# Kernel tuning notes

Measured on AMD Instinct MI355X. Metric: run time of the kernel, lower is better.

## Reference

```python
import jax, jax.numpy as jnp
import numpy as np

KH = KW = 9
BN_EPS = 1e-5


def conv3x3(x, w):
    # x: [B,Cin,H,W], w: [Cout,Cin,3,3], stride 1, padding 1
    return jax.lax.conv_general_dilated(
        x, w, window_strides=(1, 1), padding=((1, 1), (1, 1)),
        dimension_numbers=("NCHW", "OIHW", "NCHW"))


def cbr(x, w, bn):
    # bn: [4, C] rows = (gamma, beta, running_mean, running_var); inference-mode BN
    g, b, m, v = bn[0], bn[1], bn[2], bn[3]
    x = conv3x3(x, w)
    x = (x - m[:, None, None]) * (g[:, None, None] / jnp.sqrt(v[:, None, None] + BN_EPS)) + b[:, None, None]
    return jax.nn.relu(x)


def weighting(x, atten):
    # x: [B,C,H,W], atten: [B,H,W,KH*KW]
    # out[b,c,h,w] = sum_k atten[b,h,w,k] * x[b,c, h+dh(k), w+dw(k)]  (zero-padded window)
    B, C, H, W = x.shape
    patches = jax.lax.conv_general_dilated_patches(
        x, filter_shape=(KH, KW), window_strides=(1, 1),
        padding=((KH // 2, KH // 2), (KW // 2, KW // 2)))  # [B, C*KH*KW, H, W], channel-major
    patches = patches.reshape(B, C, KH * KW, H, W)
    return jnp.einsum("bckhw,bhwk->bchw", patches, atten)


def _make_params(key, fc_dim=1024):
    d4, d16 = fc_dim // 4, fc_dim // 16
    ks = jax.random.split(key, 16)
    def conv_w(k, co, ci):
        return jax.random.normal(k, (co, ci, 3, 3), jnp.float32) * (1.0 / np.sqrt(ci * 9))
    def bn(k, c):
        g = 1.0 + 0.1 * jax.random.normal(k, (c,), jnp.float32)
        return jnp.stack([g, jnp.zeros((c,)), jnp.zeros((c,)), jnp.ones((c,))])
    p = {}
    p["w1"], p["bn1"] = conv_w(ks[0], d4, fc_dim), bn(ks[1], d4)
    p["w2"], p["bn2"] = conv_w(ks[2], d16, d4), bn(ks[3], d16)
    p["w3"], p["bn3"] = conv_w(ks[4], d4, d16), bn(ks[5], d4)
    p["w4"], p["bn4"] = conv_w(ks[6], d4, fc_dim), bn(ks[7], d4)
    p["w5"], p["bn5"] = conv_w(ks[8], d4, d4), bn(ks[9], d4)
    p["fw1"] = jax.random.normal(ks[10], (10, d4), jnp.float32) * (1.0 / np.sqrt(d4))
    p["fb1"] = jnp.zeros((10,), jnp.float32)
    p["fw2"] = jax.random.normal(ks[11], (1, 10), jnp.float32) * (1.0 / np.sqrt(10))
    p["fb2"] = jnp.zeros((1,), jnp.float32)
    return p


def setup_inputs() -> dict:
    key = jax.random.key(0)
    k1, k2, k3, kp = jax.random.split(key, 4)
    B, fc_dim, H, W = 4, 1024, 64, 64
    inp = {
        "low_key": jax.random.normal(k1, (B, fc_dim, H, W), jnp.float32),
        "low_nonkey": jax.random.normal(k2, (B, fc_dim, H, W), jnp.float32),
        "local_atten": jax.random.uniform(k3, (B, H, W, KH * KW), jnp.float32),
    }
    inp.update(_make_params(kp, fc_dim))
    return inp


def reference(low_key, low_nonkey, local_atten,
              w1, bn1, w2, bn2, w3, bn3, w4, bn4, w5, bn5,
              fw1, fb1, fw2, fb2):
    x = cbr(low_key, w1, bn1)        # [B, 256, H, W]
    x = cbr(x, w2, bn2)              # [B, 64, H, W]
    x = weighting(x, local_atten)    # 9x9 local-attention weighted gather
    x = cbr(x, w3, bn3)              # [B, 256, H, W]
    y = cbr(low_nonkey, w4, bn4)     # [B, 256, H, W]
    out = cbr(x - y, w5, bn5)        # [B, 256, H, W]
    out = out.mean(axis=(2, 3))      # adaptive avg pool to 1x1 -> [B, 256]
    out = out @ fw1.T + fb1          # [B, 10]
    out = out @ fw2.T + fb2          # [B, 1]
    return out
```

## Files before the change

kernel.cpp:

```cpp
#include <hip/hip_runtime.h>
#include <math.h>

typedef _Float16 f16;
typedef f16 f16x4 __attribute__((ext_vector_type(4)));
typedef f16 f16x8 __attribute__((ext_vector_type(8)));
typedef float f32x4 __attribute__((ext_vector_type(4)));

#define NB 4

__global__ void __launch_bounds__(256)
wtrans_kernel(const float* __restrict__ w, f16* __restrict__ wt, int Co, int Cin) {
  int idx = blockIdx.x * 256 + threadIdx.x;
  int total = Co * Cin * 9;
  if (idx >= total) return;
  int ci = idx % Cin, t2 = idx / Cin;
  int co = t2 % Co, k = t2 / Co;
  wt[idx] = (f16)w[((size_t)co * Cin + ci) * 9 + k];
}

__global__ void __launch_bounds__(256)
nchw2nhwc(const float* __restrict__ in, f16* __restrict__ out) {
  __shared__ f16 s[64][66];
  const int t = threadIdx.x;
  const int bh = blockIdx.x, c0 = blockIdx.y * 64;
  const int b = bh >> 6, h = bh & 63;
  const int w = t & 63, cr = t >> 6;
  #pragma unroll
  for (int i = 0; i < 16; ++i) {
    int c = c0 + cr * 16 + i;
    s[cr * 16 + i][w] = (f16)in[(((size_t)b * 1024 + c) * 64 + h) * 64 + w];
  }
  __syncthreads();
  #pragma unroll
  for (int i = 0; i < 2; ++i) {
    int task = t + 256 * i;
    int oct = task & 7, w2 = task >> 3;
    f16x8 v;
    #pragma unroll
    for (int j = 0; j < 8; ++j) v[j] = s[oct * 8 + j][w2];
    *(f16x8*)(out + (((size_t)b * 64 + h) * 64 + w2) * 1024 + c0 + oct * 8) = v;
  }
}

__global__ void __launch_bounds__(256)
conv_mfma(const f16* __restrict__ in, const f16* __restrict__ in2,
          const f16* __restrict__ wt, const float* __restrict__ bn,
          f16* __restrict__ out, float* __restrict__ pacc,
          float* __restrict__ partial, int Cin, int Co, int kspl) {
  __shared__ __align__(16) f16 xs[6][66][40];
  __shared__ __align__(16) f16 ws[9][64][40];
  __shared__ float s_red[4][64];

  const int t = threadIdx.x;
  const int tile = blockIdx.x;
  const int b = tile >> 4;
  const int h0 = (tile & 15) * 4;
  const int co_blk = blockIdx.y * 64;
  const int ciBase = blockIdx.z * (Cin / kspl);
  const int NC = (Cin / kspl) >> 5;
  const int wid = t >> 6, lane = t & 63;
  const int l15 = lane & 15, lg = lane >> 4;
  const int koff = lg * 8;

  f32x4 acc[4][4];
  #pragma unroll
  for (int m = 0; m < 4; ++m)
    #pragma unroll
    for (int n = 0; n < 4; ++n)
      #pragma unroll
      for (int r = 0; r < 4; ++r) acc[m][n][r] = 0.f;

  const f16* inb = in + (size_t)b * Cin * 4096;
  const f16* inb2 = in2 ? in2 + (size_t)b * Cin * 4096 : nullptr;

  const int wS = t >> 2, octS = t & 3;
  f16x8 ireg[6], wreg[9];

  auto load_stage = [&](int ci0) {
    #pragma unroll
    for (int r = 0; r < 6; ++r) {
      int gh = h0 - 1 + r;
      f16x8 v = {};
      if ((unsigned)gh < 64u) {
        size_t off = ((size_t)gh * 64 + wS) * Cin + ci0 + octS * 8;
        v = *(const f16x8*)(inb + off);
        if (inb2) { f16x8 v2 = *(const f16x8*)(inb2 + off); v = v - v2; }
      }
      ireg[r] = v;
    }
    #pragma unroll
    for (int i = 0; i < 9; ++i) {
      int s = t + 256 * i;
      int oct = s & 3, co = (s >> 2) & 63, k = s >> 8;
      wreg[i] = *(const f16x8*)(wt + ((size_t)k * Co + co_blk + co) * Cin + ci0 + oct * 8);
    }
  };
  auto write_stage = [&]() {
    #pragma unroll
    for (int r = 0; r < 6; ++r)
      *(f16x8*)&xs[r][wS + 1][octS * 8] = ireg[r];
    #pragma unroll
    for (int i = 0; i < 9; ++i) {
      int s = t + 256 * i;
      int oct = s & 3, co = (s >> 2) & 63, k = s >> 8;
      *(f16x8*)&ws[k][co][oct * 8] = wreg[i];
    }
  };

  if (t < 48) {
    int r = t >> 3, side = (t >> 2) & 1, oc = t & 3;
    f16x8 z = {};
    *(f16x8*)&xs[r][side * 65][oc * 8] = z;
  }
  load_stage(ciBase);
  write_stage();
  __syncthreads();

  for (int c = 0; c < NC; ++c) {
    if (c + 1 < NC) load_stage(ciBase + ((c + 1) << 5));
    #pragma unroll
    for (int tap = 0; tap < 9; ++tap) {
      const int dh = tap / 3 - 1, dw = tap % 3 - 1;
      f16x8 af[4];
      #pragma unroll
      for (int m = 0; m < 4; ++m)
        af[m] = *(const f16x8*)&ws[tap][m * 16 + l15][koff];
      #pragma unroll
      for (int n = 0; n < 4; ++n) {
        const f16x8 bf = *(const f16x8*)&xs[wid + dh + 1][n * 16 + l15 + 1 + dw][koff];
        #pragma unroll
        for (int m = 0; m < 4; ++m)
          acc[m][n] = __builtin_amdgcn_mfma_f32_16x16x32_f16(af[m], bf, acc[m][n], 0, 0, 0);
      }
    }
    __syncthreads();
    if (c + 1 < NC) write_stage();
    __syncthreads();
  }

  if (pacc) {
    float* pb = pacc + (size_t)blockIdx.z * 4194304 + (size_t)b * 4096 * Co;
    #pragma unroll
    for (int m = 0; m < 4; ++m)
      #pragma unroll
      for (int n = 0; n < 4; ++n) {
        int px = (h0 + wid) * 64 + n * 16 + l15;
        *(f32x4*)(pb + (size_t)px * Co + co_blk + m * 16 + lg * 4) = acc[m][n];
      }
  } else if (out) {
    #pragma unroll
    for (int m = 0; m < 4; ++m) {
      float sc[4], sh[4];
      #pragma unroll
      for (int reg = 0; reg < 4; ++reg) {
        int co = co_blk + m * 16 + lg * 4 + reg;
        sc[reg] = bn[co] / sqrtf(bn[3 * Co + co] + 1e-5f);
        sh[reg] = bn[Co + co] - bn[2 * Co + co] * sc[reg];
      }
      #pragma unroll
      for (int n = 0; n < 4; ++n) {
        f16x4 v;
        #pragma unroll
        for (int reg = 0; reg < 4; ++reg)
          v[reg] = (f16)fmaxf(fmaf(acc[m][n][reg], sc[reg], sh[reg]), 0.f);
        *(f16x4*)(out + ((size_t)(b * 64 + h0 + wid) * 64 + n * 16 + l15) * Co
                      + co_blk + m * 16 + lg * 4) = v;
      }
    }
  } else {
    #pragma unroll
    for (int m = 0; m < 4; ++m)
      #pragma unroll
      for (int reg = 0; reg < 4; ++reg) {
        int co = co_blk + m * 16 + lg * 4 + reg;
        float sc = bn[co] / sqrtf(bn[3 * Co + co] + 1e-5f);
        float sh = bn[Co + co] - bn[2 * Co + co] * sc;
        float s = 0.f;
        #pragma unroll
        for (int n = 0; n < 4; ++n)
          s += fmaxf(fmaf(acc[m][n][reg], sc, sh), 0.f);
        s += __shfl_xor(s, 1, 64);
        s += __shfl_xor(s, 2, 64);
        s += __shfl_xor(s, 4, 64);
        s += __shfl_xor(s, 8, 64);
        if (l15 == 0) s_red[wid][m * 16 + lg * 4 + reg] = s;
      }
    __syncthreads();
    if (t < 64) {
      float v = s_red[0][t] + s_red[1][t] + s_red[2][t] + s_red[3][t];
      partial[((size_t)b * Co + co_blk + t) * 16 + (tile & 15)] = v;
    }
  }
}

__global__ void __launch_bounds__(256)
kreduce(const float* __restrict__ pacc, const float* __restrict__ bn,
        f16* __restrict__ out, int Co) {
  const int t = threadIdx.x;
  const int coq = t & 63;
  float sc[4], sh[4];
  #pragma unroll
  for (int r = 0; r < 4; ++r) {
    int co = coq * 4 + r;
    sc[r] = bn[co] / sqrtf(bn[3 * Co + co] + 1e-5f);
    sh[r] = bn[Co + co] - bn[2 * Co + co] * sc[r];
  }
  #pragma unroll
  for (int i = 0; i < 4; ++i) {
    size_t idx = (size_t)blockIdx.x * 1024 + i * 256 + t;
    f32x4 a = *(const f32x4*)(pacc + idx * 4);
    f32x4 b2 = *(const f32x4*)(pacc + 4194304 + idx * 4);
    f16x4 v;
    #pragma unroll
    for (int r = 0; r < 4; ++r)
      v[r] = (f16)fmaxf(fmaf(a[r] + b2[r], sc[r], sh[r]), 0.f);
    *(f16x4*)(out + idx * 4) = v;
  }
}

__global__ void __launch_bounds__(256)
weighting_nhwc(const f16* __restrict__ x, const float* __restrict__ atten,
               f16* __restrict__ out) {
  __shared__ float s_a[64 * 81];
  const int h = blockIdx.x, b = blockIdx.y;
  const int t = threadIdx.x;
  for (int idx = t; idx < 64 * 81; idx += 256)
    s_a[idx] = atten[(size_t)((b * 64 + h) * 64) * 81 + idx];
  __syncthreads();

  const int w = t & 63, cg = t >> 6;
  float acc[16];
  #pragma unroll
  for (int j = 0; j < 16; ++j) acc[j] = 0.f;

  for (int dh = -4; dh <= 4; ++dh) {
    int hh = h + dh;
    if ((unsigned)hh >= 64u) continue;
    #pragma unroll
    for (int dw = -4; dw <= 4; ++dw) {
      int ww = w + dw;
      if ((unsigned)ww >= 64u) continue;
      float a = s_a[w * 81 + (dh + 4) * 9 + (dw + 4)];
      const f16* xp = x + (((size_t)b * 64 + hh) * 64 + ww) * 64 + cg * 16;
      f16x8 v0 = *(const f16x8*)xp;
      f16x8 v1 = *(const f16x8*)(xp + 8);
      #pragma unroll
      for (int j = 0; j < 8; ++j) {
        acc[j]     = fmaf(a, (float)v0[j], acc[j]);
        acc[8 + j] = fmaf(a, (float)v1[j], acc[8 + j]);
      }
    }
  }
  f16x8 o0, o1;
  #pragma unroll
  for (int j = 0; j < 8; ++j) { o0[j] = (f16)acc[j]; o1[j] = (f16)acc[8 + j]; }
  f16* op = out + (((size_t)b * 64 + h) * 64 + w) * 64 + cg * 16;
  *(f16x8*)op = o0;
  *(f16x8*)(op + 8) = o1;
}

__global__ void __launch_bounds__(256)
fc_kernel(const float* __restrict__ partial, const float* __restrict__ fw1,
          const float* __restrict__ fb1, const float* __restrict__ fw2,
          const float* __restrict__ fb2, float* __restrict__ outp) {
  const int t = threadIdx.x;
  const int b = t >> 6, lane = t & 63;
  float pooled[4];
  #pragma unroll
  for (int k = 0; k < 4; ++k) {
    int c = lane + 64 * k;
    float s = 0.f;
    #pragma unroll
    for (int p = 0; p < 16; ++p) s += partial[(size_t)(b * 256 + c) * 16 + p];
    pooled[k] = s * (1.f / 4096.f);
  }
  float o = 0.f;
  for (int i = 0; i < 10; ++i) {
    float d = 0.f;
    #pragma unroll
    for (int k = 0; k < 4; ++k) d += pooled[k] * fw1[i * 256 + lane + 64 * k];
    #pragma unroll
    for (int off = 32; off > 0; off >>= 1) d += __shfl_down(d, off, 64);
    o += (d + fb1[i]) * fw2[i];
  }
  if (lane == 0) outp[b] = o + fb2[0];
}

extern "C" void kernel_launch(void* const* d_in, const int* in_sizes, int n_in,
                              void* d_out, int out_size, void* d_ws, size_t ws_size,
                              hipStream_t stream) {
  const float* low_key    = (const float*)d_in[0];
  const float* low_nonkey = (const float*)d_in[1];
  const float* atten      = (const float*)d_in[2];
  const float* w1 = (const float*)d_in[3];  const float* bn1 = (const float*)d_in[4];
  const float* w2 = (const float*)d_in[5];  const float* bn2 = (const float*)d_in[6];
  const float* w3 = (const float*)d_in[7];  const float* bn3 = (const float*)d_in[8];
  const float* w4 = (const float*)d_in[9];  const float* bn4 = (const float*)d_in[10];
  const float* w5 = (const float*)d_in[11]; const float* bn5 = (const float*)d_in[12];
  const float* fw1 = (const float*)d_in[13]; const float* fb1 = (const float*)d_in[14];
  const float* fw2 = (const float*)d_in[15]; const float* fb2 = (const float*)d_in[16];

  f16* T   = (f16*)d_ws;
  f16* X1  = T + 16777216;
  f16* X2  = X1 + 4194304;
  f16* X3  = X2 + 1048576;
  f16* Y   = X3 + 1048576;
  f16* wt1 = Y + 4194304;
  f16* wt2 = wt1 + 2359296;
  f16* wt3 = wt2 + 147456;
  f16* wt4 = wt3 + 147456;
  f16* wt5 = wt4 + 2359296;
  float* P    = (float*)(wt5 + 589824);
  float* Pacc = P + 16384;

  dim3 blk(256);
  wtrans_kernel<<<(256 * 1024 * 9 + 255) / 256, blk, 0, stream>>>(w1, wt1, 256, 1024);
  wtrans_kernel<<<(64 * 256 * 9 + 255) / 256, blk, 0, stream>>>(w2, wt2, 64, 256);
  wtrans_kernel<<<(256 * 64 * 9 + 255) / 256, blk, 0, stream>>>(w3, wt3, 256, 64);
  wtrans_kernel<<<(256 * 1024 * 9 + 255) / 256, blk, 0, stream>>>(w4, wt4, 256, 1024);
  wtrans_kernel<<<(256 * 256 * 9 + 255) / 256, blk, 0, stream>>>(w5, wt5, 256, 256);

  nchw2nhwc<<<dim3(256, 16), blk, 0, stream>>>(low_key, T);
  conv_mfma<<<dim3(64, 4, 2), blk, 0, stream>>>(T, nullptr, wt1, bn1, nullptr, Pacc, nullptr, 1024, 256, 2);
  kreduce<<<1024, blk, 0, stream>>>(Pacc, bn1, X1, 256);
  conv_mfma<<<dim3(64, 1, 1), blk, 0, stream>>>(X1, nullptr, wt2, bn2, X2, nullptr, nullptr, 256, 64, 1);
  weighting_nhwc<<<dim3(64, NB), blk, 0, stream>>>(X2, atten, X3);
  conv_mfma<<<dim3(64, 4, 1), blk, 0, stream>>>(X3, nullptr, wt3, bn3, X1, nullptr, nullptr, 64, 256, 1);
  nchw2nhwc<<<dim3(256, 16), blk, 0, stream>>>(low_nonkey, T);
  conv_mfma<<<dim3(64, 4, 2), blk, 0, stream>>>(T, nullptr, wt4, bn4, nullptr, Pacc, nullptr, 1024, 256, 2);
  kreduce<<<1024, blk, 0, stream>>>(Pacc, bn4, Y, 256);
  conv_mfma<<<dim3(64, 4, 1), blk, 0, stream>>>(X1, Y, wt5, bn5, nullptr, nullptr, P, 256, 256, 1);
  fc_kernel<<<1, 256, 0, stream>>>(P, fw1, fb1, fw2, fb2, (float*)d_out);
}
```

Before: 337.6 us.

## Add larger-tile split-K conv kernel for 1024-channel convs and split-K conv2

Adds a 512-thread conv kernel for the two 1024-input-channel convolutions. Each block covers 128 output channels by 8 rows and the input channels are split four ways, so each shared-memory stage is reused across more MFMAs. The 256-to-64 conv, which previously launched only 64 blocks, is also split four ways with a partial-sum reduction. kreduce is generalised to any number of slabs, and the workspace is re-laid out so the partial buffers alias the X2/X3 region. The cost is more fp32 partial-sum traffic, one block per CU with high register pressure, and a larger workspace footprint.

```diff
diff --git a/kernel.cpp b/kernel.cpp
--- a/kernel.cpp
+++ b/kernel.cpp
@@ -42,7 +42,114 @@
   }
 }
 
-__global__ void __launch_bounds__(256)
+__global__ void __launch_bounds__(512, 1)
+conv_big(const f16* __restrict__ in, const f16* __restrict__ wt,
+         float* __restrict__ pacc) {
+  constexpr int Cin = 1024, Co = 256;
+  __shared__ __align__(16) f16 xs[10][66][40];
+  __shared__ __align__(16) f16 ws[9][128][40];
+
+  const int t = threadIdx.x;
+  const int tile = blockIdx.x;
+  const int b = tile >> 3;
+  const int h0 = (tile & 7) * 8;
+  const int co_blk = blockIdx.y * 128;
+  const int ciBase = blockIdx.z * 256;
+  const int wid = t >> 6, lane = t & 63;
+  const int wave_co = wid >> 2, wave_px = wid & 3;
+  const int l15 = lane & 15, lg = lane >> 4;
+  const int koff = lg * 8;
+
+  f32x4 acc[4][8];
+  #pragma unroll
+  for (int m = 0; m < 4; ++m)
+    #pragma unroll
+    for (int n = 0; n < 8; ++n)
+      #pragma unroll
+      for (int r = 0; r < 4; ++r) acc[m][n][r] = 0.f;
+
+  const f16* inb = in + (size_t)b * Cin * 4096;
+  f16x8 ireg[5], wreg[9];
+
+  auto load_stage = [&](int ci0) {
+    #pragma unroll
+    for (int i = 0; i < 5; ++i) {
+      int task = t + 512 * i;
+      int r = task >> 8, rem = task & 255;
+      int w_ = rem >> 2, oct = rem & 3;
+      int gh = h0 - 1 + r;
+      f16x8 v = {};
+      if ((unsigned)gh < 64u)
+        v = *(const f16x8*)(inb + ((size_t)gh * 64 + w_) * Cin + ci0 + oct * 8);
+      ireg[i] = v;
+    }
+    #pragma unroll
+    for (int i = 0; i < 9; ++i) {
+      int s = t + 512 * i;
+      int oct = s & 3, co = (s >> 2) & 127, k = s >> 9;
+      wreg[i] = *(const f16x8*)(wt + ((size_t)k * Co + co_blk + co) * Cin + ci0 + oct * 8);
+    }
+  };
+  auto write_stage = [&]() {
+    #pragma unroll
+    for (int i = 0; i < 5; ++i) {
+      int task = t + 512 * i;
+      int r = task >> 8, rem = task & 255;
+      int w_ = rem >> 2, oct = rem & 3;
+      *(f16x8*)&xs[r][w_ + 1][oct * 8] = ireg[i];
+    }
+    #pragma unroll
+    for (int i = 0; i < 9; ++i) {
+      int s = t + 512 * i;
+      int oct = s & 3, co = (s >> 2) & 127, k = s >> 9;
+      *(f16x8*)&ws[k][co][oct * 8] = wreg[i];
+    }
+  };
+
+  if (t < 80) {
+    int r = t >> 3, side = (t >> 2) & 1, oc = t & 3;
+    f16x8 z = {};
+    *(f16x8*)&xs[r][side * 65][oc * 8] = z;
+  }
+  load_stage(ciBase);
+  write_stage();
+  __syncthreads();
+
+  for (int c = 0; c < 8; ++c) {
+    if (c + 1 < 8) load_stage(ciBase + ((c + 1) << 5));
+    #pragma unroll
+    for (int tap = 0; tap < 9; ++tap) {
+      const int dh = tap / 3 - 1, dw = tap % 3 - 1;
+      f16x8 af[4];
+      #pragma unroll
+      for (int m = 0; m < 4; ++m)
+        af[m] = *(const f16x8*)&ws[tap][wave_co * 64 + m * 16 + l15][koff];
+      #pragma unroll
+      for (int n = 0; n < 8; ++n) {
+        const f16x8 bf = *(const f16x8*)&xs[wave_px * 2 + (n >> 2) + dh + 1]
+                                          [(n & 3) * 16 + l15 + 1 + dw][koff];
+        #pragma unroll
+        for (int m = 0; m < 4; ++m)
+          acc[m][n] = __builtin_amdgcn_mfma_f32_16x16x32_f16(af[m], bf, acc[m][n], 0, 0, 0);
+      }
+    }
+    __syncthreads();
+    if (c + 1 < 8) write_stage();
+    __syncthreads();
+  }
+
+  float* pb = pacc + (size_t)blockIdx.z * 16384 * Co + (size_t)b * 4096 * Co;
+  #pragma unroll
+  for (int m = 0; m < 4; ++m)
+    #pragma unroll
+    for (int n = 0; n < 8; ++n) {
+      int px = (h0 + wave_px * 2 + (n >> 2)) * 64 + (n & 3) * 16 + l15;
+      int co = co_blk + wave_co * 64 + m * 16 + lg * 4;
+      *(f32x4*)(pb + (size_t)px * Co + co) = acc[m][n];
+    }
+}
+
+__global__ void __launch_bounds__(256, 1)
 conv_mfma(const f16* __restrict__ in, const f16* __restrict__ in2,
           const f16* __restrict__ wt, const float* __restrict__ bn,
           f16* __restrict__ out, float* __restrict__ pacc,
@@ -139,7 +246,7 @@
   }
 
   if (pacc) {
-    float* pb = pacc + (size_t)blockIdx.z * 4194304 + (size_t)b * 4096 * Co;
+    float* pb = pacc + (size_t)blockIdx.z * 16384 * Co + (size_t)b * 4096 * Co;
     #pragma unroll
     for (int m = 0; m < 4; ++m)
       #pragma unroll
@@ -195,13 +302,14 @@
 
 __global__ void __launch_bounds__(256)
 kreduce(const float* __restrict__ pacc, const float* __restrict__ bn,
-        f16* __restrict__ out, int Co) {
-  const int t = threadIdx.x;
-  const int coq = t & 63;
+        f16* __restrict__ out, int Co, int nslab) {
+  const int t = threadIdx.x;
+  const size_t slab = (size_t)16384 * Co;
+  const int cq = t % (Co >> 2);
   float sc[4], sh[4];
   #pragma unroll
   for (int r = 0; r < 4; ++r) {
-    int co = coq * 4 + r;
+    int co = cq * 4 + r;
     sc[r] = bn[co] / sqrtf(bn[3 * Co + co] + 1e-5f);
     sh[r] = bn[Co + co] - bn[2 * Co + co] * sc[r];
   }
@@ -209,11 +317,15 @@
   for (int i = 0; i < 4; ++i) {
     size_t idx = (size_t)blockIdx.x * 1024 + i * 256 + t;
     f32x4 a = *(const f32x4*)(pacc + idx * 4);
-    f32x4 b2 = *(const f32x4*)(pacc + 4194304 + idx * 4);
+    for (int s = 1; s < nslab; ++s) {
+      f32x4 b2 = *(const f32x4*)(pacc + slab * s + idx * 4);
+      #pragma unroll
+      for (int r = 0; r < 4; ++r) a[r] += b2[r];
+    }
     f16x4 v;
     #pragma unroll
     for (int r = 0; r < 4; ++r)
-      v[r] = (f16)fmaxf(fmaf(a[r] + b2[r], sc[r], sh[r]), 0.f);
+      v[r] = (f16)fmaxf(fmaf(a[r], sc[r], sh[r]), 0.f);
     *(f16x4*)(out + idx * 4) = v;
   }
 }
@@ -302,16 +414,17 @@
 
   f16* T   = (f16*)d_ws;
   f16* X1  = T + 16777216;
-  f16* X2  = X1 + 4194304;
-  f16* X3  = X2 + 1048576;
-  f16* Y   = X3 + 1048576;
+  f16* Y   = X1 + 4194304;
   f16* wt1 = Y + 4194304;
   f16* wt2 = wt1 + 2359296;
   f16* wt3 = wt2 + 147456;
   f16* wt4 = wt3 + 147456;
   f16* wt5 = wt4 + 2359296;
-  float* P    = (float*)(wt5 + 589824);
-  float* Pacc = P + 16384;
+  float* P  = (float*)(wt5 + 589824);
+  f16* X2   = (f16*)(P + 16384);
+  f16* X3   = X2 + 1048576;
+  float* Pacc  = (float*)X2;
+  float* Pacc2 = Pacc + 4194304;
 
   dim3 blk(256);
   wtrans_kernel<<<(256 * 1024 * 9 + 255) / 256, blk, 0, stream>>>(w1, wt1, 256, 1024);
@@ -321,14 +434,15 @@
   wtrans_kernel<<<(256 * 256 * 9 + 255) / 256, blk, 0, stream>>>(w5, wt5, 256, 256);
 
   nchw2nhwc<<<dim3(256, 16), blk, 0, stream>>>(low_key, T);
-  conv_mfma<<<dim3(64, 4, 2), blk, 0, stream>>>(T, nullptr, wt1, bn1, nullptr, Pacc, nullptr, 1024, 256, 2);
-  kreduce<<<1024, blk, 0, stream>>>(Pacc, bn1, X1, 256);
-  conv_mfma<<<dim3(64, 1, 1), blk, 0, stream>>>(X1, nullptr, wt2, bn2, X2, nullptr, nullptr, 256, 64, 1);
+  conv_big<<<dim3(32, 2, 4), dim3(512), 0, stream>>>(T, wt1, Pacc);
+  kreduce<<<1024, blk, 0, stream>>>(Pacc, bn1, X1, 256, 4);
+  conv_mfma<<<dim3(64, 1, 4), blk, 0, stream>>>(X1, nullptr, wt2, bn2, nullptr, Pacc2, nullptr, 256, 64, 4);
+  kreduce<<<256, blk, 0, stream>>>(Pacc2, bn2, X2, 64, 4);
   weighting_nhwc<<<dim3(64, NB), blk, 0, stream>>>(X2, atten, X3);
   conv_mfma<<<dim3(64, 4, 1), blk, 0, stream>>>(X3, nullptr, wt3, bn3, X1, nullptr, nullptr, 64, 256, 1);
   nchw2nhwc<<<dim3(256, 16), blk, 0, stream>>>(low_nonkey, T);
-  conv_mfma<<<dim3(64, 4, 2), blk, 0, stream>>>(T, nullptr, wt4, bn4, nullptr, Pacc, nullptr, 1024, 256, 2);
-  kreduce<<<1024, blk, 0, stream>>>(Pacc, bn4, Y, 256);
+  conv_big<<<dim3(32, 2, 4), dim3(512), 0, stream>>>(T, wt4, Pacc);
+  kreduce<<<1024, blk, 0, stream>>>(Pacc, bn4, Y, 256, 4);
   conv_mfma<<<dim3(64, 4, 1), blk, 0, stream>>>(X1, Y, wt5, bn5, nullptr, nullptr, P, 256, 256, 1);
   fc_kernel<<<1, 256, 0, stream>>>(P, fw1, fb1, fw2, fb2, (float*)d_out);
 }
```

After: 517.7 us. +53.3%, slower.
